# Kernel optimization log

Measured on AMD Instinct MI355X. Metric: run time of the kernel, lower is better.

## Reference

```python
import jax, jax.numpy as jnp
import numpy as np

# Dimensions
MAXN, MAXE = 4096, 8192
B, S, N, E = 8, 512, 1024, 2048
TYPE_DIM, MEM, TENC, EEMB, OUT = 16, 64, 32, 128, 64
MSG = TYPE_DIM + 2 * MEM + TENC + EEMB          # 304: GRU input dim
IN_GNN = EEMB + MEM                              # 192: TransformerConv in_channels
EDGE_DIM = TENC + EEMB                           # 160: TransformerConv edge_dim
# EVENT_TYPE_ID_MAP: pad=0, start=1, end=2, node-add=3, node-delete=4, edge-add=5, edge-delete=6


def setup_inputs() -> dict:
    key = jax.random.key(0)
    ks = jax.random.split(key, 32)
    ri = lambda i, shape, hi: jax.random.randint(ks[i], shape, 0, hi)
    rn = lambda i, shape, s=1.0: jax.random.normal(ks[i], shape, jnp.float32) * s
    ru = lambda i, shape: jax.random.uniform(ks[i], shape, dtype=jnp.float32)
    return {
        "event_type_ids": ri(0, (B, S), 7),
        "src_ids": ri(1, (B, S), MAXN),
        "src_mask": ru(2, (B, S)),
        "dst_ids": ri(3, (B, S), MAXN),
        "dst_mask": ru(4, (B, S)),
        "event_edge_ids": ri(5, (B, S), MAXE),
        "event_embeddings": rn(6, (B, S, EEMB)),
        "event_timestamps": ru(7, (B, S)),
        "node_ids": ri(8, (B, N), MAXN),
        "edge_ids": ri(9, (B, E), MAXE),
        "edge_index": ri(10, (B, 2, E), MAXN),
        "edge_timestamps": ru(11, (B, E)),
        "memory": rn(12, (MAXN, MEM), 0.1),
        "last_update": ru(13, (MAXE,)),
        "node_features": rn(14, (MAXN, EEMB), 0.1),
        "edge_features": rn(15, (MAXE, EEMB), 0.1),
        "type_emb": rn(16, (7, TYPE_DIM), 0.1),
        "time_w": rn(17, (TENC,), 0.1),
        "time_b": rn(18, (TENC,), 0.1),
        "gru_w_ih": rn(19, (3 * MEM, MSG), 0.05),
        "gru_w_hh": rn(20, (3 * MEM, MEM), 0.05),
        "gru_b_ih": rn(21, (3 * MEM,), 0.05),
        "gru_b_hh": rn(22, (3 * MEM,), 0.05),
        "Wq": rn(23, (OUT, IN_GNN), 0.05),
        "bq": rn(24, (OUT,), 0.05),
        "Wk": rn(25, (OUT, IN_GNN), 0.05),
        "bk": rn(26, (OUT,), 0.05),
        "Wv": rn(27, (OUT, IN_GNN), 0.05),
        "bv": rn(28, (OUT,), 0.05),
        "We": rn(29, (OUT, EDGE_DIM), 0.05),
        "Wskip": rn(30, (OUT, IN_GNN), 0.05),
        "bskip": rn(31, (OUT,), 0.05),
    }


def reference(event_type_ids, src_ids, src_mask, dst_ids, dst_mask, event_edge_ids,
              event_embeddings, event_timestamps, node_ids, edge_ids, edge_index,
              edge_timestamps, memory, last_update, node_features, edge_features,
              type_emb, time_w, time_b, gru_w_ih, gru_w_hh, gru_b_ih, gru_b_hh,
              Wq, bq, Wk, bk, Wv, bv, We, Wskip, bskip):
    f32 = jnp.float32
    time_enc = lambda t: jnp.cos(t[..., None] * time_w + time_b)  # TGN TimeEncoder: cos(Linear(t))

    # ---- message() ----
    type_embs = type_emb[event_type_ids]                      # (B,S,TYPE_DIM)
    src_embs = memory[src_ids] * src_mask[..., None]          # (B,S,MEM)
    dst_embs = memory[dst_ids] * dst_mask[..., None]
    rel_edge_ts = event_timestamps - last_update[event_edge_ids] * dst_mask
    is_node_ev = ((event_type_ids == 3) | (event_type_ids == 4)).astype(f32)
    not_special = (event_type_ids >= 3).astype(f32)           # not pad/start/end
    ts_emb = time_enc(event_timestamps * is_node_ev + rel_edge_ts * dst_mask) * not_special[..., None]
    src_msgs = jnp.concatenate([type_embs, src_embs, dst_embs, ts_emb, event_embeddings], -1) * not_special[..., None]
    dst_msgs = jnp.concatenate([type_embs, dst_embs, src_embs, ts_emb, event_embeddings], -1) * dst_mask[..., None]

    # ---- agg_message(): per-batch scatter-mean over node ids ----
    def seg_mean(m, ids):
        s = jax.ops.segment_sum(m, ids, num_segments=MAXN)
        c = jax.ops.segment_sum(jnp.ones(ids.shape, f32), ids, num_segments=MAXN)
        return s / jnp.maximum(c, 1.0)[:, None]
    # after flatten(end_dim=1), gathering by node id < MAXN picks from the batch-0 block
    agg_src0 = jax.vmap(seg_mean)(src_msgs, src_ids)[0]       # (MAXN, MSG)
    agg_dst0 = jax.vmap(seg_mean)(dst_msgs, dst_ids)[0]

    def gru(x, h):
        gi = x @ gru_w_ih.T + gru_b_ih
        gh = h @ gru_w_hh.T + gru_b_hh
        ir, iz, ic = jnp.split(gi, 3, -1)
        hr, hz, hc = jnp.split(gh, 3, -1)
        r = jax.nn.sigmoid(ir + hr)
        z = jax.nn.sigmoid(iz + hz)
        n = jnp.tanh(ic + r * hc)
        return (1.0 - z) * n + z * h

    present_src = jnp.zeros((MAXN,), bool).at[src_ids.ravel()].set(True)
    present_dst = jnp.zeros((MAXN,), bool).at[dst_ids.ravel()].set(True)
    mem_src = gru(agg_src0, memory)
    mem_dst = gru(agg_dst0, memory)
    mem = jnp.where(present_src[:, None], mem_src, memory)
    mem = jnp.where(present_dst[:, None], mem_dst, mem)

    # ---- GNN input prep ----
    rel_t_embs = time_enc(edge_timestamps - last_update[edge_ids])       # (B,E,TENC)
    x = jnp.concatenate([node_features[node_ids], mem[node_ids]], -1).reshape(B * N, IN_GNN)
    # localize_edge_index: first matching position of each edge id in flattened node_ids
    matches = node_ids.ravel()[:, None] == edge_index.ravel()[None, :]   # (B*N, B*2*E) bool
    loc = jnp.argmax(matches, axis=0).reshape(B, 2, E)                   # argmax = first True (0 if none)
    ei = loc.transpose(1, 0, 2).reshape(2, B * E)
    eattr = jnp.concatenate([rel_t_embs, edge_features[edge_ids]], -1).reshape(B * E, EDGE_DIM)

    # ---- TransformerConv (heads=1, root_weight=True, edge_dim set) ----
    q = x @ Wq.T + bq
    k = x @ Wk.T + bk
    v = x @ Wv.T + bv
    e = eattr @ We.T                                                     # lin_edge has no bias in PyG
    src, tgt = ei[0], ei[1]                                              # source_to_target flow
    k_e = k[src] + e
    v_e = v[src] + e
    score = jnp.sum(q[tgt] * k_e, -1) / np.float32(np.sqrt(OUT))
    m = jax.lax.stop_gradient(jax.ops.segment_max(score, tgt, num_segments=B * N))
    p = jnp.exp(score - m[tgt])
    den = jax.ops.segment_sum(p, tgt, num_segments=B * N)
    alpha = p / den[tgt]
    out = jax.ops.segment_sum(alpha[:, None] * v_e, tgt, num_segments=B * N)
    out = out + x @ Wskip.T + bskip
    return out.reshape(B, N, OUT)
```

## Files before the change

kernel.cpp:

```cpp
#include <hip/hip_runtime.h>
#include <math.h>

#define BB 8
#define SS 512
#define NNODE 1024
#define NEDGE 2048
#define MAXN 4096
#define MAXE 8192
#define TYPED 16
#define MEMD 64
#define TENC 32
#define EEMB 128
#define OUTD 64
#define MSG 304
#define INGNN 192
#define EDIM 160
#define BN 8192
#define BE 16384

__device__ __forceinline__ float sigmoidf(float x){ return 1.f/(1.f + expf(-x)); }

__global__ void k_init(float* zero_base, int n_zero, int* first_pos,
                       const float* Wq, const float* Wk, const float* Wv,
                       const float* Wskip, const float* We,
                       const float* bq, const float* bk,
                       const float* bv, const float* bskip,
                       float* WcatT, float* WeT, float* bcat){
  int i = blockIdx.x*blockDim.x + threadIdx.x;
  int stride = gridDim.x*blockDim.x;
  float4* z4 = (float4*)zero_base;
  int n4 = n_zero >> 2;
  float4 zero = {0.f,0.f,0.f,0.f};
  for (int t=i; t<n4; t+=stride) z4[t] = zero;
  for (int t=i; t<MAXN; t+=stride) first_pos[t] = 0x7FFFFFFF;
  int j = i;
  if (j < 4*64*192){
    int o = j/(64*192); int rem = j%(64*192); int q=rem/192, k=rem%192;
    const float* W = (o==0)?Wq:(o==1)?Wk:(o==2)?Wv:Wskip;
    WcatT[k*256 + o*64 + q] = W[rem];
  } else {
    j -= 4*64*192;
    if (j < 64*EDIM){ int q=j/EDIM, k=j%EDIM; WeT[k*64+q] = We[j]; }
    else {
      j -= 64*EDIM;
      if (j < 256){
        const float* b = (j<64)?bq:(j<128)?bk:(j<192)?bv:bskip;
        bcat[j] = b[j&63];
      }
    }
  }
}

__global__ void k_msg_first(const int* ev_type, const int* src_ids, const float* src_mask,
                            const int* dst_ids, const float* dst_mask, const int* ev_edge,
                            const float* ev_emb, const float* ev_ts, const float* memory,
                            const float* last_update, const float* type_emb,
                            const float* time_w, const float* time_b,
                            float* agg_src, float* agg_dst, int* cnt_src, int* cnt_dst,
                            const int* node_ids, int* first_pos, int* ps, int* pd){
  int bb = blockIdx.x;
  if (bb < SS){
    int s = bb;
    int et = ev_type[s];
    int sid = src_ids[s], did = dst_ids[s];
    float sm = src_mask[s], dm = dst_mask[s];
    float ts = ev_ts[s];
    float ns = (et >= 3) ? 1.f : 0.f;
    float ine = (et == 3 || et == 4) ? 1.f : 0.f;
    float rel = ts - last_update[ev_edge[s]] * dm;
    float tin = ts*ine + rel*dm;
    int d = threadIdx.x;
    if (d < MSG){
      float vs, vd;
      if (d < TYPED){ float t = type_emb[et*TYPED + d]; vs = t; vd = t; }
      else if (d < 80){ int c=d-16;  vs = memory[sid*MEMD+c]*sm; vd = memory[did*MEMD+c]*dm; }
      else if (d < 144){ int c=d-80; vs = memory[did*MEMD+c]*dm; vd = memory[sid*MEMD+c]*sm; }
      else if (d < 176){ int c=d-144; float ce = cosf(tin*time_w[c]+time_b[c])*ns; vs=ce; vd=ce; }
      else { float e = ev_emb[s*EEMB + (d-176)]; vs=e; vd=e; }
      atomicAdd(&agg_src[sid*MSG+d], vs*ns);
      atomicAdd(&agg_dst[did*MSG+d], vd*dm);
    }
    if (d == MSG){ atomicAdd(&cnt_src[sid], 1); atomicAdd(&cnt_dst[did], 1); }
  } else {
    int i = (bb - SS)*320 + threadIdx.x;
    if (i < BN) atomicMin(&first_pos[node_ids[i]], i);
    if (i < BB*SS){ ps[src_ids[i]] = 1; pd[dst_ids[i]] = 1; }
  }
}

#define GNT 8
#define GPAD 12
__global__ __launch_bounds__(192) void k_gru(
    const float* agg_src, const float* agg_dst, const int* cnt_src, const int* cnt_dst,
    const int* ps, const int* pd, const float* memory,
    const float* w_ih, const float* w_hh, const float* b_ih, const float* b_hh,
    float* mem_new){
  __shared__ float xs_t[MSG][GPAD];
  __shared__ float hs_t[MEMD][GPAD];
  __shared__ float giL[GNT][192];
  __shared__ float ghL[GNT][192];
  __shared__ int   mode[GNT];
  __shared__ float rcnt[GNT];
  int tid = threadIdx.x;
  int base = blockIdx.x * GNT;
  if (tid < GNT){
    int n = base + tid;
    int m = pd[n] ? 2 : (ps[n] ? 1 : 0);
    mode[tid] = m;
    int c = (m==2) ? cnt_dst[n] : ((m==1) ? cnt_src[n] : 0);
    rcnt[tid] = 1.f / (float)max(c, 1);
  }
  __syncthreads();
  for (int idx = tid; idx < GNT*MSG; idx += 192){
    int t = idx / MSG, k = idx - t*MSG;
    const float* agg = (mode[t]==2) ? agg_dst : agg_src;
    xs_t[k][t] = agg[(base+t)*MSG + k] * rcnt[t];
  }
  for (int idx = tid; idx < GNT*MEMD; idx += 192){
    int t = idx / MEMD, k = idx - t*MEMD;
    hs_t[k][t] = memory[(base+t)*MEMD + k];
  }
  __syncthreads();
  {
    float4 a0 = {0.f,0.f,0.f,0.f}, a1 = {0.f,0.f,0.f,0.f};
    const float* wr = &w_ih[tid*MSG];
    #pragma unroll 2
    for (int k4 = 0; k4 < MSG; k4 += 4){
      float4 w4 = *(const float4*)&wr[k4];
      {
        float4 x0 = *(const float4*)&xs_t[k4][0];
        float4 x1 = *(const float4*)&xs_t[k4][4];
        a0.x += w4.x*x0.x; a0.y += w4.x*x0.y; a0.z += w4.x*x0.z; a0.w += w4.x*x0.w;
        a1.x += w4.x*x1.x; a1.y += w4.x*x1.y; a1.z += w4.x*x1.z; a1.w += w4.x*x1.w;
      }
      {
        float4 x0 = *(const float4*)&xs_t[k4+1][0];
        float4 x1 = *(const float4*)&xs_t[k4+1][4];
        a0.x += w4.y*x0.x; a0.y += w4.y*x0.y; a0.z += w4.y*x0.z; a0.w += w4.y*x0.w;
        a1.x += w4.y*x1.x; a1.y += w4.y*x1.y; a1.z += w4.y*x1.z; a1.w += w4.y*x1.w;
      }
      {
        float4 x0 = *(const float4*)&xs_t[k4+2][0];
        float4 x1 = *(const float4*)&xs_t[k4+2][4];
        a0.x += w4.z*x0.x; a0.y += w4.z*x0.y; a0.z += w4.z*x0.z; a0.w += w4.z*x0.w;
        a1.x += w4.z*x1.x; a1.y += w4.z*x1.y; a1.z += w4.z*x1.z; a1.w += w4.z*x1.w;
      }
      {
        float4 x0 = *(const float4*)&xs_t[k4+3][0];
        float4 x1 = *(const float4*)&xs_t[k4+3][4];
        a0.x += w4.w*x0.x; a0.y += w4.w*x0.y; a0.z += w4.w*x0.z; a0.w += w4.w*x0.w;
        a1.x += w4.w*x1.x; a1.y += w4.w*x1.y; a1.z += w4.w*x1.z; a1.w += w4.w*x1.w;
      }
    }
    float bi = b_ih[tid];
    giL[0][tid]=a0.x+bi; giL[1][tid]=a0.y+bi; giL[2][tid]=a0.z+bi; giL[3][tid]=a0.w+bi;
    giL[4][tid]=a1.x+bi; giL[5][tid]=a1.y+bi; giL[6][tid]=a1.z+bi; giL[7][tid]=a1.w+bi;
  }
  {
    float4 a0 = {0.f,0.f,0.f,0.f}, a1 = {0.f,0.f,0.f,0.f};
    const float* wr = &w_hh[tid*MEMD];
    #pragma unroll 2
    for (int k4 = 0; k4 < MEMD; k4 += 4){
      float4 w4 = *(const float4*)&wr[k4];
      {
        float4 x0 = *(const float4*)&hs_t[k4][0];
        float4 x1 = *(const float4*)&hs_t[k4][4];
        a0.x += w4.x*x0.x; a0.y += w4.x*x0.y; a0.z += w4.x*x0.z; a0.w += w4.x*x0.w;
        a1.x += w4.x*x1.x; a1.y += w4.x*x1.y; a1.z += w4.x*x1.z; a1.w += w4.x*x1.w;
      }
      {
        float4 x0 = *(const float4*)&hs_t[k4+1][0];
        float4 x1 = *(const float4*)&hs_t[k4+1][4];
        a0.x += w4.y*x0.x; a0.y += w4.y*x0.y; a0.z += w4.y*x0.z; a0.w += w4.y*x0.w;
        a1.x += w4.y*x1.x; a1.y += w4.y*x1.y; a1.z += w4.y*x1.z; a1.w += w4.y*x1.w;
      }
      {
        float4 x0 = *(const float4*)&hs_t[k4+2][0];
        float4 x1 = *(const float4*)&hs_t[k4+2][4];
        a0.x += w4.z*x0.x; a0.y += w4.z*x0.y; a0.z += w4.z*x0.z; a0.w += w4.z*x0.w;
        a1.x += w4.z*x1.x; a1.y += w4.z*x1.y; a1.z += w4.z*x1.z; a1.w += w4.z*x1.w;
      }
      {
        float4 x0 = *(const float4*)&hs_t[k4+3][0];
        float4 x1 = *(const float4*)&hs_t[k4+3][4];
        a0.x += w4.w*x0.x; a0.y += w4.w*x0.y; a0.z += w4.w*x0.z; a0.w += w4.w*x0.w;
        a1.x += w4.w*x1.x; a1.y += w4.w*x1.y; a1.z += w4.w*x1.z; a1.w += w4.w*x1.w;
      }
    }
    float bh = b_hh[tid];
    ghL[0][tid]=a0.x+bh; ghL[1][tid]=a0.y+bh; ghL[2][tid]=a0.z+bh; ghL[3][tid]=a0.w+bh;
    ghL[4][tid]=a1.x+bh; ghL[5][tid]=a1.y+bh; ghL[6][tid]=a1.z+bh; ghL[7][tid]=a1.w+bh;
  }
  __syncthreads();
  int cw = tid >> 6, col = tid & 63;
  for (int t = cw; t < GNT; t += 3){
    float h = hs_t[col][t];
    float outv;
    if (mode[t] == 0) outv = h;
    else {
      float r  = sigmoidf(giL[t][col]     + ghL[t][col]);
      float z  = sigmoidf(giL[t][64+col]  + ghL[t][64+col]);
      float ng = tanhf  (giL[t][128+col] + r*ghL[t][128+col]);
      outv = (1.f - z)*ng + z*h;
    }
    mem_new[(base+t)*MEMD + col] = outv;
  }
}

#define QK_CH 96
#define EE_CH 80
__global__ __launch_bounds__(256) void k_mm(
    const int* node_ids, const float* node_feat, const float* mem_new,
    const float* WcatT, const float* bcat,
    float* qbuf, float* kbuf, float* vbuf, float* outbuf,
    const int* edge_ids, const float* edge_ts, const float* last_update,
    const float* edge_features, const float* time_w, const float* time_b,
    const float* WeT, float* ebuf){
  __shared__ float smem[QK_CH*68 + QK_CH*64];
  int tid = threadIdx.x;
  if (blockIdx.x < 512){
    float* xs_t = smem;
    float* wls  = smem + QK_CH*68;
    int rg = blockIdx.x >> 2, cg = blockIdx.x & 3;
    int rbase = rg * 64;
    int rr = tid & 63, qq = tid >> 6;
    int nid = node_ids[rbase + rr];
    int tr = tid >> 4, tc = tid & 15;
    float4 acc[4];
    #pragma unroll
    for (int i=0;i<4;i++) acc[i] = (float4){0.f,0.f,0.f,0.f};
    for (int kc = 0; kc < 2; kc++){
      #pragma unroll 6
      for (int m = 0; m < 24; m++){
        int kk = qq*24 + m;
        int k  = kc*QK_CH + kk;
        float v = (k < EEMB) ? node_feat[nid*EEMB + k] : mem_new[nid*MEMD + (k-EEMB)];
        xs_t[kk*68 + rr] = v;
      }
      #pragma unroll
      for (int it = 0; it < 6; it++){
        int idx = tid + it*256;
        int kk = idx >> 4, c4 = (idx & 15) * 4;
        *(float4*)&wls[kk*64 + c4] = *(const float4*)&WcatT[(kc*QK_CH + kk)*256 + cg*64 + c4];
      }
      __syncthreads();
      #pragma unroll 4
      for (int kk = 0; kk < QK_CH; kk++){
        float4 xv = *(const float4*)&xs_t[kk*68 + tr*4];
        float4 wv = *(const float4*)&wls[kk*64 + tc*4];
        acc[0].x += xv.x*wv.x; acc[0].y += xv.x*wv.y; acc[0].z += xv.x*wv.z; acc[0].w += xv.x*wv.w;
        acc[1].x += xv.y*wv.x; acc[1].y += xv.y*wv.y; acc[1].z += xv.y*wv.z; acc[1].w += xv.y*wv.w;
        acc[2].x += xv.z*wv.x; acc[2].y += xv.z*wv.y; acc[2].z += xv.z*wv.z; acc[2].w += xv.z*wv.w;
        acc[3].x += xv.w*wv.x; acc[3].y += xv.w*wv.y; acc[3].z += xv.w*wv.z; acc[3].w += xv.w*wv.w;
      }
      __syncthreads();
    }
    float4 b4 = *(const float4*)&bcat[cg*64 + tc*4];
    float* dst = (cg==0)? qbuf : (cg==1)? kbuf : (cg==2)? vbuf : outbuf;
    #pragma unroll
    for (int i=0;i<4;i++){
      float4 o = {acc[i].x+b4.x, acc[i].y+b4.y, acc[i].z+b4.z, acc[i].w+b4.w};
      *(float4*)&dst[(rbase + tr*4 + i)*OUTD + tc*4] = o;
    }
  } else {
    float* ea_t = smem;
    float* wls  = smem + EE_CH*68;
    int ebase = (blockIdx.x - 512) * 64;
    int ee = tid & 63, qq = tid >> 6;
    int j = ebase + ee;
    int eid = edge_ids[j];
    float rel = edge_ts[j] - last_update[eid];
    int tr = tid >> 4, tc = tid & 15;
    float4 acc[4];
    #pragma unroll
    for (int i=0;i<4;i++) acc[i] = (float4){0.f,0.f,0.f,0.f};
    for (int kc = 0; kc < 2; kc++){
      #pragma unroll 5
      for (int m = 0; m < 20; m++){
        int kk = qq*20 + m;
        int k  = kc*EE_CH + kk;
        float v = (k < TENC) ? cosf(rel*time_w[k] + time_b[k])
                             : edge_features[eid*EEMB + (k - TENC)];
        ea_t[kk*68 + ee] = v;
      }
      #pragma unroll
      for (int it = 0; it < 5; it++){
        int idx = tid + it*256;
        int kk = idx >> 4, c4 = (idx & 15) * 4;
        *(float4*)&wls[kk*64 + c4] = *(const float4*)&WeT[(kc*EE_CH + kk)*64 + c4];
      }
      __syncthreads();
      #pragma unroll 4
      for (int kk = 0; kk < EE_CH; kk++){
        float4 ev = *(const float4*)&ea_t[kk*68 + tr*4];
        float4 wv = *(const float4*)&wls[kk*64 + tc*4];
        acc[0].x += ev.x*wv.x; acc[0].y += ev.x*wv.y; acc[0].z += ev.x*wv.z; acc[0].w += ev.x*wv.w;
        acc[1].x += ev.y*wv.x; acc[1].y += ev.y*wv.y; acc[1].z += ev.y*wv.z; acc[1].w += ev.y*wv.w;
        acc[2].x += ev.z*wv.x; acc[2].y += ev.z*wv.y; acc[2].z += ev.z*wv.z; acc[2].w += ev.z*wv.w;
        acc[3].x += ev.w*wv.x; acc[3].y += ev.w*wv.y; acc[3].z += ev.w*wv.z; acc[3].w += ev.w*wv.w;
      }
      __syncthreads();
    }
    #pragma unroll
    for (int i=0;i<4;i++)
      *(float4*)&ebuf[(ebase + tr*4 + i)*OUTD + tc*4] = acc[i];
  }
}

__global__ void k_score(const int* edge_index, const int* first_pos,
                        const float* qbuf, const float* kbuf, const float* ebuf,
                        float* pbuf, int* srcpos, int* tgtpos,
                        float* den, float* den0part){
  __shared__ float sden[4];
  int w = threadIdx.x >> 6;
  int j = blockIdx.x*4 + w;
  int c = threadIdx.x & 63;
  int b = j / NEDGE, e = j % NEDGE;
  int vsrc = edge_index[b*2*NEDGE + e];
  int vtgt = edge_index[b*2*NEDGE + NEDGE + e];
  int fs = first_pos[vsrc]; if (fs == 0x7FFFFFFF) fs = 0;
  int ft = first_pos[vtgt]; if (ft == 0x7FFFFFFF) ft = 0;
  float partial = qbuf[ft*OUTD + c] * (kbuf[fs*OUTD + c] + ebuf[j*OUTD + c]);
  #pragma unroll
  for (int off=32; off>0; off>>=1) partial += __shfl_down(partial, off, 64);
  if (c == 0){
    float score = partial * 0.125f;
    float p = expf(score);
    pbuf[j] = p;
    srcpos[j] = fs; tgtpos[j] = ft;
    sden[w] = (ft == 0) ? p : 0.f;
    if (ft != 0) atomicAdd(&den[ft], p);
  }
  __syncthreads();
  if (threadIdx.x == 0) den0part[blockIdx.x] = sden[0]+sden[1]+sden[2]+sden[3];
}

__global__ __launch_bounds__(1024) void k_out(const int* srcpos, const int* tgtpos,
                                              const float* pbuf, const float* den,
                                              const float* vbuf, const float* ebuf,
                                              float* out, float* out0part){
  __shared__ float acc0[16][64];
  int tid = threadIdx.x;
  int w = tid >> 6, c = tid & 63;
  int jbase = blockIdx.x*64 + w*4;
  float a0 = 0.f;
  #pragma unroll
  for (int i=0;i<4;i++){
    int j = jbase + i;
    int ft = tgtpos[j], fs = srcpos[j];
    float p = pbuf[j];
    float ve = vbuf[fs*OUTD + c] + ebuf[j*OUTD + c];
    if (ft == 0) a0 += p * ve;
    else atomicAdd(&out[ft*OUTD + c], (p/den[ft]) * ve);
  }
  acc0[w][c] = a0;
  __syncthreads();
  if (w == 0){
    float t = 0.f;
    #pragma unroll
    for (int i=0;i<16;i++) t += acc0[i][c];
    out0part[blockIdx.x*64 + c] = t;
  }
}

__global__ __launch_bounds__(1024) void k_fin_out(const float* den0part,
                                                  const float* out0part, float* out){
  __shared__ float part[16][64];
  __shared__ float dpart[16];
  __shared__ float s_inv;
  int tid = threadIdx.x;
  int w = tid >> 6, c = tid & 63;
  float d = den0part[tid] + den0part[tid+1024] + den0part[tid+2048] + den0part[tid+3072];
  #pragma unroll
  for (int off=32; off>0; off>>=1) d += __shfl_down(d, off, 64);
  if (c == 0) dpart[w] = d;
  float s = 0.f;
  #pragma unroll
  for (int i=0;i<16;i++) s += out0part[(w + i*16)*64 + c];
  part[w][c] = s;
  __syncthreads();
  if (tid == 0){
    float dt = 0.f;
    #pragma unroll
    for (int i=0;i<16;i++) dt += dpart[i];
    s_inv = (dt > 0.f) ? 1.f/dt : 0.f;
  }
  __syncthreads();
  if (w == 0){
    float t = 0.f;
    #pragma unroll
    for (int i=0;i<16;i++) t += part[i][c];
    out[c] += t * s_inv;
  }
}

extern "C" void kernel_launch(void* const* d_in, const int* in_sizes, int n_in,
                              void* d_out, int out_size, void* d_ws, size_t ws_size,
                              hipStream_t stream){
  const int*   ev_type      = (const int*)  d_in[0];
  const int*   src_ids      = (const int*)  d_in[1];
  const float* src_mask     = (const float*)d_in[2];
  const int*   dst_ids      = (const int*)  d_in[3];
  const float* dst_mask     = (const float*)d_in[4];
  const int*   ev_edge      = (const int*)  d_in[5];
  const float* ev_emb       = (const float*)d_in[6];
  const float* ev_ts        = (const float*)d_in[7];
  const int*   node_ids     = (const int*)  d_in[8];
  const int*   edge_ids     = (const int*)  d_in[9];
  const int*   edge_index   = (const int*)  d_in[10];
  const float* edge_ts      = (const float*)d_in[11];
  const float* memory       = (const float*)d_in[12];
  const float* last_update  = (const float*)d_in[13];
  const float* node_feat    = (const float*)d_in[14];
  const float* edge_feat    = (const float*)d_in[15];
  const float* type_emb     = (const float*)d_in[16];
  const float* time_w       = (const float*)d_in[17];
  const float* time_b       = (const float*)d_in[18];
  const float* gru_w_ih     = (const float*)d_in[19];
  const float* gru_w_hh     = (const float*)d_in[20];
  const float* gru_b_ih     = (const float*)d_in[21];
  const float* gru_b_hh     = (const float*)d_in[22];
  const float* Wq  = (const float*)d_in[23]; const float* bq    = (const float*)d_in[24];
  const float* Wk  = (const float*)d_in[25]; const float* bk    = (const float*)d_in[26];
  const float* Wv  = (const float*)d_in[27]; const float* bv    = (const float*)d_in[28];
  const float* We  = (const float*)d_in[29];
  const float* Wsk = (const float*)d_in[30]; const float* bskip = (const float*)d_in[31];
  float* out = (float*)d_out;

  float* ws = (float*)d_ws;
  size_t off = 0;
  float* agg_src = ws + off; off += (size_t)MAXN*MSG;
  float* agg_dst = ws + off; off += (size_t)MAXN*MSG;
  int* cnt_src   = (int*)(ws + off); off += MAXN;
  int* cnt_dst   = (int*)(ws + off); off += MAXN;
  int* present_s = (int*)(ws + off); off += MAXN;
  int* present_d = (int*)(ws + off); off += MAXN;
  float* den     = ws + off; off += BN;
  int n_zero = (int)off;
  int* first_pos = (int*)(ws + off); off += MAXN;
  float* mem_new = ws + off; off += (size_t)MAXN*MEMD;
  float* qbuf    = ws + off; off += (size_t)BN*OUTD;
  float* kbuf    = ws + off; off += (size_t)BN*OUTD;
  float* vbuf    = ws + off; off += (size_t)BN*OUTD;
  float* ebuf    = ws + off; off += (size_t)BE*OUTD;
  float* pbuf    = ws + off; off += BE;
  int* srcpos    = (int*)(ws + off); off += BE;
  int* tgtpos    = (int*)(ws + off); off += BE;
  float* den0part= ws + off; off += 4096;
  float* out0part= ws + off; off += 256*64;
  float* WcatT   = ws + off; off += (size_t)INGNN*256;
  float* WeT     = ws + off; off += (size_t)EDIM*64;
  float* bcat    = ws + off; off += 256;

  k_init<<<2048, 256, 0, stream>>>(ws, n_zero, first_pos,
                                   Wq, Wk, Wv, Wsk, We, bq, bk, bv, bskip,
                                   WcatT, WeT, bcat);
  k_msg_first<<<SS + (BN + 319)/320, 320, 0, stream>>>(
      ev_type, src_ids, src_mask, dst_ids, dst_mask, ev_edge,
      ev_emb, ev_ts, memory, last_update, type_emb, time_w, time_b,
      agg_src, agg_dst, cnt_src, cnt_dst,
      node_ids, first_pos, present_s, present_d);
  k_gru<<<MAXN/GNT, 192, 0, stream>>>(agg_src, agg_dst, cnt_src, cnt_dst,
                                      present_s, present_d, memory,
                                      gru_w_ih, gru_w_hh, gru_b_ih, gru_b_hh, mem_new);
  k_mm<<<512 + BE/64, 256, 0, stream>>>(node_ids, node_feat, mem_new, WcatT, bcat,
                                        qbuf, kbuf, vbuf, out,
                                        edge_ids, edge_ts, last_update, edge_feat,
                                        time_w, time_b, WeT, ebuf);
  k_score<<<BE/4, 256, 0, stream>>>(edge_index, first_pos, qbuf, kbuf, ebuf,
                                    pbuf, srcpos, tgtpos, den, den0part);
  k_out<<<256, 1024, 0, stream>>>(srcpos, tgtpos, pbuf, den, vbuf, ebuf, out, out0part);
  k_fin_out<<<1, 1024, 0, stream>>>(den0part, out0part, out);
}
```

Measured before the change: 83.97 us.

## Fuse all stages into one cooperative persistent kernel with grid syncs

Replaces the seven-kernel launch chain with a single cooperative kernel of 256 blocks that runs init, message aggregation, GRU, projections, scoring and output phases separated by grid-wide syncs. The score stage now accumulates softmax numerators and denominators directly with atomics into a zeroed num buffer, so the separate output-gather kernel is no longer needed. The aim is to remove kernel launch gaps and one full pass over edges, at the cost of lower parallelism per phase, a larger zeroing region, and grid-sync overhead. The old kernels remain as a fallback if cooperative launch fails.

```diff
diff --git a/kernel.cpp b/kernel.cpp
--- a/kernel.cpp
+++ b/kernel.cpp
@@ -1,5 +1,8 @@
 #include <hip/hip_runtime.h>
+#include <hip/hip_cooperative_groups.h>
 #include <math.h>
+
+namespace cg = cooperative_groups;
 
 #define BB 8
 #define SS 512
@@ -18,9 +21,351 @@
 #define BN 8192
 #define BE 16384
 
+#define GRID 256
+#define TPB 256
+#define QK_CH 96
+#define EE_CH 80
+
 __device__ __forceinline__ float sigmoidf(float x){ return 1.f/(1.f + expf(-x)); }
 
-__global__ void k_init(float* zero_base, int n_zero, int* first_pos,
+struct TgnArgs {
+  const int *ev_type, *src_ids, *dst_ids, *ev_edge, *node_ids, *edge_ids, *edge_index;
+  const float *src_mask, *dst_mask, *ev_emb, *ev_ts, *edge_ts, *memory, *last_update,
+              *node_feat, *edge_feat, *type_emb, *time_w, *time_b,
+              *w_ih, *w_hh, *b_ih, *b_hh,
+              *Wq, *bq, *Wk, *bk, *Wv, *bv, *We, *Wskip, *bskip;
+  float *out;
+  float *agg_src, *agg_dst;
+  int *cnt_src, *cnt_dst, *ps, *pd, *first_pos;
+  float *den, *num, *mem_new, *qbuf, *kbuf, *vbuf, *ebuf,
+        *den0part, *out0part, *WcatT, *WeT, *bcat, *zero_base;
+  int n_zero4;
+};
+
+__global__ __launch_bounds__(TPB) void k_all(TgnArgs A){
+  cg::grid_group grid = cg::this_grid();
+  __shared__ float smem[QK_CH*68 + QK_CH*64];
+  int blk = blockIdx.x, tid = threadIdx.x;
+  int gid = blk*TPB + tid;
+
+  {
+    float4* z4 = (float4*)A.zero_base;
+    float4 zz = {0.f,0.f,0.f,0.f};
+    for (int t = gid; t < A.n_zero4; t += GRID*TPB) z4[t] = zz;
+    for (int t = gid; t < MAXN; t += GRID*TPB) A.first_pos[t] = 0x7FFFFFFF;
+    const int NT1 = 4*64*192, NT2 = 64*EDIM;
+    for (int j = gid; j < NT1 + NT2 + 256; j += GRID*TPB){
+      int jj = j;
+      if (jj < NT1){
+        int o = jj/(64*192); int rem = jj%(64*192); int q = rem/192, k = rem%192;
+        const float* W = (o==0)?A.Wq:(o==1)?A.Wk:(o==2)?A.Wv:A.Wskip;
+        A.WcatT[k*256 + o*64 + q] = W[rem];
+      } else {
+        jj -= NT1;
+        if (jj < NT2){ int q = jj/EDIM, k = jj%EDIM; A.WeT[k*64+q] = A.We[jj]; }
+        else {
+          jj -= NT2;
+          const float* b = (jj<64)?A.bq:(jj<128)?A.bk:(jj<192)?A.bv:A.bskip;
+          A.bcat[jj] = b[jj&63];
+        }
+      }
+    }
+  }
+  grid.sync();
+
+  {
+    for (int s = blk; s < SS; s += GRID){
+      int et = A.ev_type[s];
+      int sid = A.src_ids[s], did = A.dst_ids[s];
+      float sm = A.src_mask[s], dm = A.dst_mask[s];
+      float ts = A.ev_ts[s];
+      float ns = (et >= 3) ? 1.f : 0.f;
+      float ine = (et == 3 || et == 4) ? 1.f : 0.f;
+      float rel = ts - A.last_update[A.ev_edge[s]] * dm;
+      float tin = ts*ine + rel*dm;
+      for (int d = tid; d < MSG; d += TPB){
+        float vs, vd;
+        if (d < TYPED){ float t = A.type_emb[et*TYPED + d]; vs = t; vd = t; }
+        else if (d < 80){ int c=d-16;  vs = A.memory[sid*MEMD+c]*sm; vd = A.memory[did*MEMD+c]*dm; }
+        else if (d < 144){ int c=d-80; vs = A.memory[did*MEMD+c]*dm; vd = A.memory[sid*MEMD+c]*sm; }
+        else if (d < 176){ int c=d-144; float ce = cosf(tin*A.time_w[c]+A.time_b[c])*ns; vs=ce; vd=ce; }
+        else { float e = A.ev_emb[s*EEMB + (d-176)]; vs=e; vd=e; }
+        atomicAdd(&A.agg_src[sid*MSG+d], vs*ns);
+        atomicAdd(&A.agg_dst[did*MSG+d], vd*dm);
+      }
+      if (tid == 0){ atomicAdd(&A.cnt_src[sid], 1); atomicAdd(&A.cnt_dst[did], 1); }
+    }
+    for (int i = gid; i < BN; i += GRID*TPB){
+      atomicMin(&A.first_pos[A.node_ids[i]], i);
+      if (i < BB*SS){ A.ps[A.src_ids[i]] = 1; A.pd[A.dst_ids[i]] = 1; }
+    }
+  }
+  grid.sync();
+
+  for (int base = blk*8; base < MAXN; base += GRID*8){
+    float* xs_t = smem;
+    float* hs_t = smem + 3648;
+    float* giL  = smem + 4416;
+    float* ghL  = smem + 5952;
+    int*   mode = (int*)(smem + 7488);
+    float* rcnt = smem + 7496;
+    if (tid < 8){
+      int n = base + tid;
+      int m = A.pd[n] ? 2 : (A.ps[n] ? 1 : 0);
+      mode[tid] = m;
+      int c = (m==2) ? A.cnt_dst[n] : ((m==1) ? A.cnt_src[n] : 0);
+      rcnt[tid] = 1.f / (float)max(c, 1);
+    }
+    __syncthreads();
+    for (int idx = tid; idx < 8*MSG; idx += TPB){
+      int t = idx / MSG, k = idx - t*MSG;
+      const float* agg = (mode[t]==2) ? A.agg_dst : A.agg_src;
+      xs_t[k*12 + t] = agg[(base+t)*MSG + k] * rcnt[t];
+    }
+    for (int idx = tid; idx < 8*MEMD; idx += TPB){
+      int t = idx / MEMD, k = idx - t*MEMD;
+      hs_t[k*12 + t] = A.memory[(base+t)*MEMD + k];
+    }
+    __syncthreads();
+    if (tid < 192){
+      float4 a0={0,0,0,0}, a1={0,0,0,0};
+      const float* wr = &A.w_ih[tid*MSG];
+      #pragma unroll 2
+      for (int k4 = 0; k4 < MSG; k4 += 4){
+        float4 w4 = *(const float4*)&wr[k4];
+        float4 x0, x1;
+        x0 = *(const float4*)&xs_t[(k4+0)*12]; x1 = *(const float4*)&xs_t[(k4+0)*12+4];
+        a0.x += w4.x*x0.x; a0.y += w4.x*x0.y; a0.z += w4.x*x0.z; a0.w += w4.x*x0.w;
+        a1.x += w4.x*x1.x; a1.y += w4.x*x1.y; a1.z += w4.x*x1.z; a1.w += w4.x*x1.w;
+        x0 = *(const float4*)&xs_t[(k4+1)*12]; x1 = *(const float4*)&xs_t[(k4+1)*12+4];
+        a0.x += w4.y*x0.x; a0.y += w4.y*x0.y; a0.z += w4.y*x0.z; a0.w += w4.y*x0.w;
+        a1.x += w4.y*x1.x; a1.y += w4.y*x1.y; a1.z += w4.y*x1.z; a1.w += w4.y*x1.w;
+        x0 = *(const float4*)&xs_t[(k4+2)*12]; x1 = *(const float4*)&xs_t[(k4+2)*12+4];
+        a0.x += w4.z*x0.x; a0.y += w4.z*x0.y; a0.z += w4.z*x0.z; a0.w += w4.z*x0.w;
+        a1.x += w4.z*x1.x; a1.y += w4.z*x1.y; a1.z += w4.z*x1.z; a1.w += w4.z*x1.w;
+        x0 = *(const float4*)&xs_t[(k4+3)*12]; x1 = *(const float4*)&xs_t[(k4+3)*12+4];
+        a0.x += w4.w*x0.x; a0.y += w4.w*x0.y; a0.z += w4.w*x0.z; a0.w += w4.w*x0.w;
+        a1.x += w4.w*x1.x; a1.y += w4.w*x1.y; a1.z += w4.w*x1.z; a1.w += w4.w*x1.w;
+      }
+      float bi = A.b_ih[tid];
+      giL[0*192+tid]=a0.x+bi; giL[1*192+tid]=a0.y+bi; giL[2*192+tid]=a0.z+bi; giL[3*192+tid]=a0.w+bi;
+      giL[4*192+tid]=a1.x+bi; giL[5*192+tid]=a1.y+bi; giL[6*192+tid]=a1.z+bi; giL[7*192+tid]=a1.w+bi;
+      float4 b0={0,0,0,0}, b1={0,0,0,0};
+      const float* wh = &A.w_hh[tid*MEMD];
+      #pragma unroll 2
+      for (int k4 = 0; k4 < MEMD; k4 += 4){
+        float4 w4 = *(const float4*)&wh[k4];
+        float4 x0, x1;
+        x0 = *(const float4*)&hs_t[(k4+0)*12]; x1 = *(const float4*)&hs_t[(k4+0)*12+4];
+        b0.x += w4.x*x0.x; b0.y += w4.x*x0.y; b0.z += w4.x*x0.z; b0.w += w4.x*x0.w;
+        b1.x += w4.x*x1.x; b1.y += w4.x*x1.y; b1.z += w4.x*x1.z; b1.w += w4.x*x1.w;
+        x0 = *(const float4*)&hs_t[(k4+1)*12]; x1 = *(const float4*)&hs_t[(k4+1)*12+4];
+        b0.x += w4.y*x0.x; b0.y += w4.y*x0.y; b0.z += w4.y*x0.z; b0.w += w4.y*x0.w;
+        b1.x += w4.y*x1.x; b1.y += w4.y*x1.y; b1.z += w4.y*x1.z; b1.w += w4.y*x1.w;
+        x0 = *(const float4*)&hs_t[(k4+2)*12]; x1 = *(const float4*)&hs_t[(k4+2)*12+4];
+        b0.x += w4.z*x0.x; b0.y += w4.z*x0.y; b0.z += w4.z*x0.z; b0.w += w4.z*x0.w;
+        b1.x += w4.z*x1.x; b1.y += w4.z*x1.y; b1.z += w4.z*x1.z; b1.w += w4.z*x1.w;
+        x0 = *(const float4*)&hs_t[(k4+3)*12]; x1 = *(const float4*)&hs_t[(k4+3)*12+4];
+        b0.x += w4.w*x0.x; b0.y += w4.w*x0.y; b0.z += w4.w*x0.z; b0.w += w4.w*x0.w;
+        b1.x += w4.w*x1.x; b1.y += w4.w*x1.y; b1.z += w4.w*x1.z; b1.w += w4.w*x1.w;
+      }
+      float bh = A.b_hh[tid];
+      ghL[0*192+tid]=b0.x+bh; ghL[1*192+tid]=b0.y+bh; ghL[2*192+tid]=b0.z+bh; ghL[3*192+tid]=b0.w+bh;
+      ghL[4*192+tid]=b1.x+bh; ghL[5*192+tid]=b1.y+bh; ghL[6*192+tid]=b1.z+bh; ghL[7*192+tid]=b1.w+bh;
+    }
+    __syncthreads();
+    int cw = tid >> 6, col = tid & 63;
+    for (int t = cw; t < 8; t += 4){
+      float h = hs_t[col*12 + t];
+      float outv;
+      int m = mode[t];
+      if (m == 0) outv = h;
+      else {
+        float r  = sigmoidf(giL[t*192+col]      + ghL[t*192+col]);
+        float z  = sigmoidf(giL[t*192+64+col]   + ghL[t*192+64+col]);
+        float ng = tanhf  (giL[t*192+128+col] + r*ghL[t*192+128+col]);
+        outv = (1.f - z)*ng + z*h;
+      }
+      A.mem_new[(base+t)*MEMD + col] = outv;
+    }
+    __syncthreads();
+  }
+  grid.sync();
+
+  for (int unit = blk; unit < 768; unit += GRID){
+    if (unit < 512){
+      float* xs_t = smem;
+      float* wls  = smem + QK_CH*68;
+      int rg = unit >> 2, cgx = unit & 3;
+      int rbase = rg * 64;
+      int rr = tid & 63, qq = tid >> 6;
+      int nid = A.node_ids[rbase + rr];
+      int tr = tid >> 4, tc = tid & 15;
+      float4 acc[4];
+      #pragma unroll
+      for (int i=0;i<4;i++) acc[i] = (float4){0.f,0.f,0.f,0.f};
+      for (int kc = 0; kc < 2; kc++){
+        #pragma unroll 6
+        for (int m = 0; m < 24; m++){
+          int kk = qq*24 + m;
+          int k  = kc*QK_CH + kk;
+          float v = (k < EEMB) ? A.node_feat[nid*EEMB + k] : A.mem_new[nid*MEMD + (k-EEMB)];
+          xs_t[kk*68 + rr] = v;
+        }
+        #pragma unroll
+        for (int it = 0; it < 6; it++){
+          int idx = tid + it*256;
+          int kk = idx >> 4, c4 = (idx & 15) * 4;
+          *(float4*)&wls[kk*64 + c4] = *(const float4*)&A.WcatT[(kc*QK_CH + kk)*256 + cgx*64 + c4];
+        }
+        __syncthreads();
+        #pragma unroll 4
+        for (int kk = 0; kk < QK_CH; kk++){
+          float4 xv = *(const float4*)&xs_t[kk*68 + tr*4];
+          float4 wv = *(const float4*)&wls[kk*64 + tc*4];
+          acc[0].x += xv.x*wv.x; acc[0].y += xv.x*wv.y; acc[0].z += xv.x*wv.z; acc[0].w += xv.x*wv.w;
+          acc[1].x += xv.y*wv.x; acc[1].y += xv.y*wv.y; acc[1].z += xv.y*wv.z; acc[1].w += xv.y*wv.w;
+          acc[2].x += xv.z*wv.x; acc[2].y += xv.z*wv.y; acc[2].z += xv.z*wv.z; acc[2].w += xv.z*wv.w;
+          acc[3].x += xv.w*wv.x; acc[3].y += xv.w*wv.y; acc[3].z += xv.w*wv.z; acc[3].w += xv.w*wv.w;
+        }
+        __syncthreads();
+      }
+      float4 b4 = *(const float4*)&A.bcat[cgx*64 + tc*4];
+      float* dst = (cgx==0)? A.qbuf : (cgx==1)? A.kbuf : (cgx==2)? A.vbuf : A.out;
+      #pragma unroll
+      for (int i=0;i<4;i++){
+        float4 o = {acc[i].x+b4.x, acc[i].y+b4.y, acc[i].z+b4.z, acc[i].w+b4.w};
+        *(float4*)&dst[(rbase + tr*4 + i)*OUTD + tc*4] = o;
+      }
+    } else {
+      float* ea_t = smem;
+      float* wls  = smem + EE_CH*68;
+      int ebase = (unit - 512) * 64;
+      int ee = tid & 63, qq = tid >> 6;
+      int j = ebase + ee;
+      int eid = A.edge_ids[j];
+      float rel = A.edge_ts[j] - A.last_update[eid];
+      int tr = tid >> 4, tc = tid & 15;
+      float4 acc[4];
+      #pragma unroll
+      for (int i=0;i<4;i++) acc[i] = (float4){0.f,0.f,0.f,0.f};
+      for (int kc = 0; kc < 2; kc++){
+        #pragma unroll 5
+        for (int m = 0; m < 20; m++){
+          int kk = qq*20 + m;
+          int k  = kc*EE_CH + kk;
+          float v = (k < TENC) ? cosf(rel*A.time_w[k] + A.time_b[k])
+                               : A.edge_feat[eid*EEMB + (k - TENC)];
+          ea_t[kk*68 + ee] = v;
+        }
+        #pragma unroll
+        for (int it = 0; it < 5; it++){
+          int idx = tid + it*256;
+          int kk = idx >> 4, c4 = (idx & 15) * 4;
+          *(float4*)&wls[kk*64 + c4] = *(const float4*)&A.WeT[(kc*EE_CH + kk)*64 + c4];
+        }
+        __syncthreads();
+        #pragma unroll 4
+        for (int kk = 0; kk < EE_CH; kk++){
+          float4 ev = *(const float4*)&ea_t[kk*68 + tr*4];
+          float4 wv = *(const float4*)&wls[kk*64 + tc*4];
+          acc[0].x += ev.x*wv.x; acc[0].y += ev.x*wv.y; acc[0].z += ev.x*wv.z; acc[0].w += ev.x*wv.w;
+          acc[1].x += ev.y*wv.x; acc[1].y += ev.y*wv.y; acc[1].z += ev.y*wv.z; acc[1].w += ev.y*wv.w;
+          acc[2].x += ev.z*wv.x; acc[2].y += ev.z*wv.y; acc[2].z += ev.z*wv.z; acc[2].w += ev.z*wv.w;
+          acc[3].x += ev.w*wv.x; acc[3].y += ev.w*wv.y; acc[3].z += ev.w*wv.z; acc[3].w += ev.w*wv.w;
+        }
+        __syncthreads();
+      }
+      #pragma unroll
+      for (int i=0;i<4;i++)
+        *(float4*)&A.ebuf[(ebase + tr*4 + i)*OUTD + tc*4] = acc[i];
+    }
+  }
+  grid.sync();
+
+  {
+    float* acc0 = smem;
+    float* sdw  = smem + 256;
+    int w = tid >> 6, c = tid & 63;
+    for (int chunk = blk; chunk < 1024; chunk += GRID){
+      float a0 = 0.f, pden = 0.f;
+      #pragma unroll
+      for (int u = 0; u < 4; u++){
+        int j = chunk*16 + w*4 + u;
+        int b = j >> 11, e = j & 2047;
+        int vsrc = A.edge_index[b*2*NEDGE + e];
+        int vtgt = A.edge_index[b*2*NEDGE + NEDGE + e];
+        int fs = A.first_pos[vsrc]; if (fs == 0x7FFFFFFF) fs = 0;
+        int ft = A.first_pos[vtgt]; if (ft == 0x7FFFFFFF) ft = 0;
+        float ej = A.ebuf[j*OUTD + c];
+        float partial = A.qbuf[ft*OUTD + c] * (A.kbuf[fs*OUTD + c] + ej);
+        #pragma unroll
+        for (int off = 32; off > 0; off >>= 1) partial += __shfl_down(partial, off, 64);
+        float sc = __shfl(partial, 0, 64);
+        float pe = expf(sc * 0.125f);
+        float ve = A.vbuf[fs*OUTD + c] + ej;
+        if (ft == 0){ a0 += pe*ve; pden += pe; }
+        else {
+          atomicAdd(&A.num[ft*OUTD + c], pe*ve);
+          if (c == 0) atomicAdd(&A.den[ft], pe);
+        }
+      }
+      acc0[w*64 + c] = a0;
+      if (c == 0) sdw[w] = pden;
+      __syncthreads();
+      if (w == 0){
+        float t4 = acc0[c] + acc0[64+c] + acc0[128+c] + acc0[192+c];
+        A.out0part[chunk*64 + c] = t4;
+        if (c == 0) A.den0part[chunk] = sdw[0]+sdw[1]+sdw[2]+sdw[3];
+      }
+      __syncthreads();
+    }
+  }
+  grid.sync();
+
+  for (int unit = blk; unit < 516; unit += GRID){
+    if (unit < 512){
+      int r = unit*16 + (tid >> 4);
+      int c4 = (tid & 15) * 4;
+      if (r > 0){
+        float d = A.den[r];
+        if (d > 0.f){
+          float rinv = 1.f / d;
+          float4 n4 = *(const float4*)&A.num[r*64 + c4];
+          float4 o4 = *(const float4*)&A.out[r*64 + c4];
+          o4.x += n4.x*rinv; o4.y += n4.y*rinv; o4.z += n4.z*rinv; o4.w += n4.w*rinv;
+          *(float4*)&A.out[r*64 + c4] = o4;
+        }
+      }
+    } else {
+      float* sdata = smem;
+      float* dred  = smem + 256;
+      int cbase = (unit - 512) * 16;
+      int ci = tid >> 4, ch = tid & 15;
+      int c = cbase + ci;
+      float s = 0.f;
+      for (int j = ch*64; j < ch*64 + 64; j++) s += A.out0part[j*64 + c];
+      sdata[ci*16 + ch] = s;
+      float dd = A.den0part[tid] + A.den0part[tid+256] + A.den0part[tid+512] + A.den0part[tid+768];
+      #pragma unroll
+      for (int off = 32; off > 0; off >>= 1) dd += __shfl_down(dd, off, 64);
+      if ((tid & 63) == 0) dred[tid >> 6] = dd;
+      __syncthreads();
+      if (tid == 0) smem[260] = dred[0]+dred[1]+dred[2]+dred[3];
+      __syncthreads();
+      if (ch == 0){
+        float den0 = smem[260];
+        float tot = 0.f;
+        #pragma unroll
+        for (int q = 0; q < 16; q++) tot += sdata[ci*16 + q];
+        if (den0 > 0.f) A.out[c] += tot / den0;
+      }
+      __syncthreads();
+    }
+  }
+}
+
+__global__ void f_init(float* zero_base, int n_zero, int* first_pos,
                        const float* Wq, const float* Wk, const float* Wv,
                        const float* Wskip, const float* We,
                        const float* bq, const float* bk,
@@ -51,7 +396,7 @@
   }
 }
 
-__global__ void k_msg_first(const int* ev_type, const int* src_ids, const float* src_mask,
+__global__ void f_msg_first(const int* ev_type, const int* src_ids, const float* src_mask,
                             const int* dst_ids, const float* dst_mask, const int* ev_edge,
                             const float* ev_emb, const float* ev_ts, const float* memory,
                             const float* last_update, const float* type_emb,
@@ -89,14 +434,13 @@
 }
 
 #define GNT 8
-#define GPAD 12
-__global__ __launch_bounds__(192) void k_gru(
+__global__ __launch_bounds__(192) void f_gru(
     const float* agg_src, const float* agg_dst, const int* cnt_src, const int* cnt_dst,
     const int* ps, const int* pd, const float* memory,
     const float* w_ih, const float* w_hh, const float* b_ih, const float* b_hh,
     float* mem_new){
-  __shared__ float xs_t[MSG][GPAD];
-  __shared__ float hs_t[MEMD][GPAD];
+  __shared__ float xs_t[MSG][12];
+  __shared__ float hs_t[MEMD][12];
   __shared__ float giL[GNT][192];
   __shared__ float ghL[GNT][192];
   __shared__ int   mode[GNT];
@@ -122,70 +466,48 @@
   }
   __syncthreads();
   {
-    float4 a0 = {0.f,0.f,0.f,0.f}, a1 = {0.f,0.f,0.f,0.f};
+    float4 a0 = {0,0,0,0}, a1 = {0,0,0,0};
     const float* wr = &w_ih[tid*MSG];
     #pragma unroll 2
     for (int k4 = 0; k4 < MSG; k4 += 4){
       float4 w4 = *(const float4*)&wr[k4];
-      {
-        float4 x0 = *(const float4*)&xs_t[k4][0];
-        float4 x1 = *(const float4*)&xs_t[k4][4];
-        a0.x += w4.x*x0.x; a0.y += w4.x*x0.y; a0.z += w4.x*x0.z; a0.w += w4.x*x0.w;
-        a1.x += w4.x*x1.x; a1.y += w4.x*x1.y; a1.z += w4.x*x1.z; a1.w += w4.x*x1.w;
-      }
-      {
-        float4 x0 = *(const float4*)&xs_t[k4+1][0];
-        float4 x1 = *(const float4*)&xs_t[k4+1][4];
-        a0.x += w4.y*x0.x; a0.y += w4.y*x0.y; a0.z += w4.y*x0.z; a0.w += w4.y*x0.w;
-        a1.x += w4.y*x1.x; a1.y += w4.y*x1.y; a1.z += w4.y*x1.z; a1.w += w4.y*x1.w;
-      }
-      {
-        float4 x0 = *(const float4*)&xs_t[k4+2][0];
-        float4 x1 = *(const float4*)&xs_t[k4+2][4];
-        a0.x += w4.z*x0.x; a0.y += w4.z*x0.y; a0.z += w4.z*x0.z; a0.w += w4.z*x0.w;
-        a1.x += w4.z*x1.x; a1.y += w4.z*x1.y; a1.z += w4.z*x1.z; a1.w += w4.z*x1.w;
-      }
-      {
-        float4 x0 = *(const float4*)&xs_t[k4+3][0];
-        float4 x1 = *(const float4*)&xs_t[k4+3][4];
-        a0.x += w4.w*x0.x; a0.y += w4.w*x0.y; a0.z += w4.w*x0.z; a0.w += w4.w*x0.w;
-        a1.x += w4.w*x1.x; a1.y += w4.w*x1.y; a1.z += w4.w*x1.z; a1.w += w4.w*x1.w;
-      }
+      float4 x0, x1;
+      x0 = *(const float4*)&xs_t[k4+0][0]; x1 = *(const float4*)&xs_t[k4+0][4];
+      a0.x += w4.x*x0.x; a0.y += w4.x*x0.y; a0.z += w4.x*x0.z; a0.w += w4.x*x0.w;
+      a1.x += w4.x*x1.x; a1.y += w4.x*x1.y; a1.z += w4.x*x1.z; a1.w += w4.x*x1.w;
+      x0 = *(const float4*)&xs_t[k4+1][0]; x1 = *(const float4*)&xs_t[k4+1][4];
+      a0.x += w4.y*x0.x; a0.y += w4.y*x0.y; a0.z += w4.y*x0.z; a0.w += w4.y*x0.w;
+      a1.x += w4.y*x1.x; a1.y += w4.y*x1.y; a1.z += w4.y*x1.z; a1.w += w4.y*x1.w;
+      x0 = *(const float4*)&xs_t[k4+2][0]; x1 = *(const float4*)&xs_t[k4+2][4];
+      a0.x += w4.z*x0.x; a0.y += w4.z*x0.y; a0.z += w4.z*x0.z; a0.w += w4.z*x0.w;
+      a1.x += w4.z*x1.x; a1.y += w4.z*x1.y; a1.z += w4.z*x1.z; a1.w += w4.z*x1.w;
+      x0 = *(const float4*)&xs_t[k4+3][0]; x1 = *(const float4*)&xs_t[k4+3][4];
+      a0.x += w4.w*x0.x; a0.y += w4.w*x0.y; a0.z += w4.w*x0.z; a0.w += w4.w*x0.w;
+      a1.x += w4.w*x1.x; a1.y += w4.w*x1.y; a1.z += w4.w*x1.z; a1.w += w4.w*x1.w;
     }
     float bi = b_ih[tid];
     giL[0][tid]=a0.x+bi; giL[1][tid]=a0.y+bi; giL[2][tid]=a0.z+bi; giL[3][tid]=a0.w+bi;
     giL[4][tid]=a1.x+bi; giL[5][tid]=a1.y+bi; giL[6][tid]=a1.z+bi; giL[7][tid]=a1.w+bi;
   }
   {
-    float4 a0 = {0.f,0.f,0.f,0.f}, a1 = {0.f,0.f,0.f,0.f};
+    float4 a0 = {0,0,0,0}, a1 = {0,0,0,0};
     const float* wr = &w_hh[tid*MEMD];
     #pragma unroll 2
     for (int k4 = 0; k4 < MEMD; k4 += 4){
       float4 w4 = *(const float4*)&wr[k4];
-      {
-        float4 x0 = *(const float4*)&hs_t[k4][0];
-        float4 x1 = *(const float4*)&hs_t[k4][4];
-        a0.x += w4.x*x0.x; a0.y += w4.x*x0.y; a0.z += w4.x*x0.z; a0.w += w4.x*x0.w;
-        a1.x += w4.x*x1.x; a1.y += w4.x*x1.y; a1.z += w4.x*x1.z; a1.w += w4.x*x1.w;
-      }
-      {
-        float4 x0 = *(const float4*)&hs_t[k4+1][0];
-        float4 x1 = *(const float4*)&hs_t[k4+1][4];
-        a0.x += w4.y*x0.x; a0.y += w4.y*x0.y; a0.z += w4.y*x0.z; a0.w += w4.y*x0.w;
-        a1.x += w4.y*x1.x; a1.y += w4.y*x1.y; a1.z += w4.y*x1.z; a1.w += w4.y*x1.w;
-      }
-      {
-        float4 x0 = *(const float4*)&hs_t[k4+2][0];
-        float4 x1 = *(const float4*)&hs_t[k4+2][4];
-        a0.x += w4.z*x0.x; a0.y += w4.z*x0.y; a0.z += w4.z*x0.z; a0.w += w4.z*x0.w;
-        a1.x += w4.z*x1.x; a1.y += w4.z*x1.y; a1.z += w4.z*x1.z; a1.w += w4.z*x1.w;
-      }
-      {
-        float4 x0 = *(const float4*)&hs_t[k4+3][0];
-        float4 x1 = *(const float4*)&hs_t[k4+3][4];
-        a0.x += w4.w*x0.x; a0.y += w4.w*x0.y; a0.z += w4.w*x0.z; a0.w += w4.w*x0.w;
-        a1.x += w4.w*x1.x; a1.y += w4.w*x1.y; a1.z += w4.w*x1.z; a1.w += w4.w*x1.w;
-      }
+      float4 x0, x1;
+      x0 = *(const float4*)&hs_t[k4+0][0]; x1 = *(const float4*)&hs_t[k4+0][4];
+      a0.x += w4.x*x0.x; a0.y += w4.x*x0.y; a0.z += w4.x*x0.z; a0.w += w4.x*x0.w;
+      a1.x += w4.x*x1.x; a1.y += w4.x*x1.y; a1.z += w4.x*x1.z; a1.w += w4.x*x1.w;
+      x0 = *(const float4*)&hs_t[k4+1][0]; x1 = *(const float4*)&hs_t[k4+1][4];
+      a0.x += w4.y*x0.x; a0.y += w4.y*x0.y; a0.z += w4.y*x0.z; a0.w += w4.y*x0.w;
+      a1.x += w4.y*x1.x; a1.y += w4.y*x1.y; a1.z += w4.y*x1.z; a1.w += w4.y*x1.w;
+      x0 = *(const float4*)&hs_t[k4+2][0]; x1 = *(const float4*)&hs_t[k4+2][4];
+      a0.x += w4.z*x0.x; a0.y += w4.z*x0.y; a0.z += w4.z*x0.z; a0.w += w4.z*x0.w;
+      a1.x += w4.z*x1.x; a1.y += w4.z*x1.y; a1.z += w4.z*x1.z; a1.w += w4.z*x1.w;
+      x0 = *(const float4*)&hs_t[k4+3][0]; x1 = *(const float4*)&hs_t[k4+3][4];
+      a0.x += w4.w*x0.x; a0.y += w4.w*x0.y; a0.z += w4.w*x0.z; a0.w += w4.w*x0.w;
+      a1.x += w4.w*x1.x; a1.y += w4.w*x1.y; a1.z += w4.w*x1.z; a1.w += w4.w*x1.w;
     }
     float bh = b_hh[tid];
     ghL[0][tid]=a0.x+bh; ghL[1][tid]=a0.y+bh; ghL[2][tid]=a0.z+bh; ghL[3][tid]=a0.w+bh;
@@ -207,9 +529,7 @@
   }
 }
 
-#define QK_CH 96
-#define EE_CH 80
-__global__ __launch_bounds__(256) void k_mm(
+__global__ __launch_bounds__(256) void f_mm(
     const int* node_ids, const float* node_feat, const float* mem_new,
     const float* WcatT, const float* bcat,
     float* qbuf, float* kbuf, float* vbuf, float* outbuf,
@@ -221,7 +541,7 @@
   if (blockIdx.x < 512){
     float* xs_t = smem;
     float* wls  = smem + QK_CH*68;
-    int rg = blockIdx.x >> 2, cg = blockIdx.x & 3;
+    int rg = blockIdx.x >> 2, cgx = blockIdx.x & 3;
     int rbase = rg * 64;
     int rr = tid & 63, qq = tid >> 6;
     int nid = node_ids[rbase + rr];
@@ -241,7 +561,7 @@
       for (int it = 0; it < 6; it++){
         int idx = tid + it*256;
         int kk = idx >> 4, c4 = (idx & 15) * 4;
-        *(float4*)&wls[kk*64 + c4] = *(const float4*)&WcatT[(kc*QK_CH + kk)*256 + cg*64 + c4];
+        *(float4*)&wls[kk*64 + c4] = *(const float4*)&WcatT[(kc*QK_CH + kk)*256 + cgx*64 + c4];
       }
       __syncthreads();
       #pragma unroll 4
@@ -255,8 +575,8 @@
       }
       __syncthreads();
     }
-    float4 b4 = *(const float4*)&bcat[cg*64 + tc*4];
-    float* dst = (cg==0)? qbuf : (cg==1)? kbuf : (cg==2)? vbuf : outbuf;
+    float4 b4 = *(const float4*)&bcat[cgx*64 + tc*4];
+    float* dst = (cgx==0)? qbuf : (cgx==1)? kbuf : (cgx==2)? vbuf : outbuf;
     #pragma unroll
     for (int i=0;i<4;i++){
       float4 o = {acc[i].x+b4.x, acc[i].y+b4.y, acc[i].z+b4.z, acc[i].w+b4.w};
@@ -307,7 +627,7 @@
   }
 }
 
-__global__ void k_score(const int* edge_index, const int* first_pos,
+__global__ void f_score(const int* edge_index, const int* first_pos,
                         const float* qbuf, const float* kbuf, const float* ebuf,
                         float* pbuf, int* srcpos, int* tgtpos,
                         float* den, float* den0part){
@@ -335,7 +655,7 @@
   if (threadIdx.x == 0) den0part[blockIdx.x] = sden[0]+sden[1]+sden[2]+sden[3];
 }
 
-__global__ __launch_bounds__(1024) void k_out(const int* srcpos, const int* tgtpos,
+__global__ __launch_bounds__(1024) void f_out(const int* srcpos, const int* tgtpos,
                                               const float* pbuf, const float* den,
                                               const float* vbuf, const float* ebuf,
                                               float* out, float* out0part){
@@ -363,7 +683,7 @@
   }
 }
 
-__global__ __launch_bounds__(1024) void k_fin_out(const float* den0part,
+__global__ __launch_bounds__(1024) void f_fin_out(const float* den0part,
                                                   const float* out0part, float* out){
   __shared__ float part[16][64];
   __shared__ float dpart[16];
@@ -397,78 +717,91 @@
 extern "C" void kernel_launch(void* const* d_in, const int* in_sizes, int n_in,
                               void* d_out, int out_size, void* d_ws, size_t ws_size,
                               hipStream_t stream){
-  const int*   ev_type      = (const int*)  d_in[0];
-  const int*   src_ids      = (const int*)  d_in[1];
-  const float* src_mask     = (const float*)d_in[2];
-  const int*   dst_ids      = (const int*)  d_in[3];
-  const float* dst_mask     = (const float*)d_in[4];
-  const int*   ev_edge      = (const int*)  d_in[5];
-  const float* ev_emb       = (const float*)d_in[6];
-  const float* ev_ts        = (const float*)d_in[7];
-  const int*   node_ids     = (const int*)  d_in[8];
-  const int*   edge_ids     = (const int*)  d_in[9];
-  const int*   edge_index   = (const int*)  d_in[10];
-  const float* edge_ts      = (const float*)d_in[11];
-  const float* memory       = (const float*)d_in[12];
-  const float* last_update  = (const float*)d_in[13];
-  const float* node_feat    = (const float*)d_in[14];
-  const float* edge_feat    = (const float*)d_in[15];
-  const float* type_emb     = (const float*)d_in[16];
-  const float* time_w       = (const float*)d_in[17];
-  const float* time_b       = (const float*)d_in[18];
-  const float* gru_w_ih     = (const float*)d_in[19];
-  const float* gru_w_hh     = (const float*)d_in[20];
-  const float* gru_b_ih     = (const float*)d_in[21];
-  const float* gru_b_hh     = (const float*)d_in[22];
-  const float* Wq  = (const float*)d_in[23]; const float* bq    = (const float*)d_in[24];
-  const float* Wk  = (const float*)d_in[25]; const float* bk    = (const float*)d_in[26];
-  const float* Wv  = (const float*)d_in[27]; const float* bv    = (const float*)d_in[28];
-  const float* We  = (const float*)d_in[29];
-  const float* Wsk = (const float*)d_in[30]; const float* bskip = (const float*)d_in[31];
-  float* out = (float*)d_out;
+  TgnArgs A;
+  A.ev_type     = (const int*)  d_in[0];
+  A.src_ids     = (const int*)  d_in[1];
+  A.src_mask    = (const float*)d_in[2];
+  A.dst_ids     = (const int*)  d_in[3];
+  A.dst_mask    = (const float*)d_in[4];
+  A.ev_edge     = (const int*)  d_in[5];
+  A.ev_emb      = (const float*)d_in[6];
+  A.ev_ts       = (const float*)d_in[7];
+  A.node_ids    = (const int*)  d_in[8];
+  A.edge_ids    = (const int*)  d_in[9];
+  A.edge_index  = (const int*)  d_in[10];
+  A.edge_ts     = (const float*)d_in[11];
+  A.memory      = (const float*)d_in[12];
+  A.last_update = (const float*)d_in[13];
+  A.node_feat   = (const float*)d_in[14];
+  A.edge_feat   = (const float*)d_in[15];
+  A.type_emb    = (const float*)d_in[16];
+  A.time_w      = (const float*)d_in[17];
+  A.time_b      = (const float*)d_in[18];
+  A.w_ih        = (const float*)d_in[19];
+  A.w_hh        = (const float*)d_in[20];
+  A.b_ih        = (const float*)d_in[21];
+  A.b_hh        = (const float*)d_in[22];
+  A.Wq = (const float*)d_in[23]; A.bq = (const float*)d_in[24];
+  A.Wk = (const float*)d_in[25]; A.bk = (const float*)d_in[26];
+  A.Wv = (const float*)d_in[27]; A.bv = (const float*)d_in[28];
+  A.We = (const float*)d_in[29];
+  A.Wskip = (const float*)d_in[30]; A.bskip = (const float*)d_in[31];
+  A.out = (float*)d_out;
 
   float* ws = (float*)d_ws;
   size_t off = 0;
-  float* agg_src = ws + off; off += (size_t)MAXN*MSG;
-  float* agg_dst = ws + off; off += (size_t)MAXN*MSG;
-  int* cnt_src   = (int*)(ws + off); off += MAXN;
-  int* cnt_dst   = (int*)(ws + off); off += MAXN;
-  int* present_s = (int*)(ws + off); off += MAXN;
-  int* present_d = (int*)(ws + off); off += MAXN;
-  float* den     = ws + off; off += BN;
+  A.zero_base = ws;
+  A.agg_src = ws + off; off += (size_t)MAXN*MSG;
+  A.agg_dst = ws + off; off += (size_t)MAXN*MSG;
+  A.cnt_src = (int*)(ws + off); off += MAXN;
+  A.cnt_dst = (int*)(ws + off); off += MAXN;
+  A.ps      = (int*)(ws + off); off += MAXN;
+  A.pd      = (int*)(ws + off); off += MAXN;
+  A.den     = ws + off; off += BN;
+  A.num     = ws + off; off += (size_t)BN*OUTD;
   int n_zero = (int)off;
-  int* first_pos = (int*)(ws + off); off += MAXN;
-  float* mem_new = ws + off; off += (size_t)MAXN*MEMD;
-  float* qbuf    = ws + off; off += (size_t)BN*OUTD;
-  float* kbuf    = ws + off; off += (size_t)BN*OUTD;
-  float* vbuf    = ws + off; off += (size_t)BN*OUTD;
-  float* ebuf    = ws + off; off += (size_t)BE*OUTD;
-  float* pbuf    = ws + off; off += BE;
-  int* srcpos    = (int*)(ws + off); off += BE;
-  int* tgtpos    = (int*)(ws + off); off += BE;
-  float* den0part= ws + off; off += 4096;
-  float* out0part= ws + off; off += 256*64;
-  float* WcatT   = ws + off; off += (size_t)INGNN*256;
-  float* WeT     = ws + off; off += (size_t)EDIM*64;
-  float* bcat    = ws + off; off += 256;
-
-  k_init<<<2048, 256, 0, stream>>>(ws, n_zero, first_pos,
-                                   Wq, Wk, Wv, Wsk, We, bq, bk, bv, bskip,
-                                   WcatT, WeT, bcat);
-  k_msg_first<<<SS + (BN + 319)/320, 320, 0, stream>>>(
-      ev_type, src_ids, src_mask, dst_ids, dst_mask, ev_edge,
-      ev_emb, ev_ts, memory, last_update, type_emb, time_w, time_b,
-      agg_src, agg_dst, cnt_src, cnt_dst,
-      node_ids, first_pos, present_s, present_d);
-  k_gru<<<MAXN/GNT, 192, 0, stream>>>(agg_src, agg_dst, cnt_src, cnt_dst,
-                                      present_s, present_d, memory,
-                                      gru_w_ih, gru_w_hh, gru_b_ih, gru_b_hh, mem_new);
-  k_mm<<<512 + BE/64, 256, 0, stream>>>(node_ids, node_feat, mem_new, WcatT, bcat,
-                                        qbuf, kbuf, vbuf, out,
-                                        edge_ids, edge_ts, last_update, edge_feat,
-                                        time_w, time_b, WeT, ebuf);
-  k_score<<<BE/4, 256, 0, stream>>>(edge_index, first_pos, qbuf, kbuf, ebuf,
-                                    pbuf, srcpos, tgtpos, den, den0part);
-  k_out<<<256, 1024, 0, stream>>>(srcpos, tgtpos, pbuf, den, vbuf, ebuf, out, out0part);
-  k_fin_out<<<1, 1024, 0, stream>>>(den0part, out0part, out);
+  A.n_zero4 = n_zero >> 2;
+  A.first_pos = (int*)(ws + off); off += MAXN;
+  A.mem_new   = ws + off; off += (size_t)MAXN*MEMD;
+  A.qbuf      = ws + off; off += (size_t)BN*OUTD;
+  A.kbuf      = ws + off; off += (size_t)BN*OUTD;
+  A.vbuf      = ws + off; off += (size_t)BN*OUTD;
+  A.ebuf      = ws + off; off += (size_t)BE*OUTD;
+  A.den0part  = ws + off; off += 1024;
+  A.out0part  = ws + off; off += 1024*64;
+  float* pbuf      = ws + off; off += BE;
+  int*   srcpos    = (int*)(ws + off); off += BE;
+  int*   tgtpos    = (int*)(ws + off); off += BE;
+  float* den0part7 = ws + off; off += 4096;
+  float* out0part7 = ws + off; off += 256*64;
+  A.WcatT     = ws + off; off += (size_t)INGNN*256;
+  A.WeT       = ws + off; off += (size_t)EDIM*64;
+  A.bcat      = ws + off; off += 256;
+
+  void* args[] = { (void*)&A };
+  hipError_t err = hipLaunchCooperativeKernel((const void*)k_all, dim3(GRID), dim3(TPB),
+                                              args, 0, stream);
+  if (err != hipSuccess){
+    f_init<<<2048, 256, 0, stream>>>(ws, n_zero, A.first_pos,
+                                     A.Wq, A.Wk, A.Wv, A.Wskip, A.We,
+                                     A.bq, A.bk, A.bv, A.bskip,
+                                     A.WcatT, A.WeT, A.bcat);
+    f_msg_first<<<SS + (BN + 319)/320, 320, 0, stream>>>(
+        A.ev_type, A.src_ids, A.src_mask, A.dst_ids, A.dst_mask, A.ev_edge,
+        A.ev_emb, A.ev_ts, A.memory, A.last_update, A.type_emb, A.time_w, A.time_b,
+        A.agg_src, A.agg_dst, A.cnt_src, A.cnt_dst,
+        A.node_ids, A.first_pos, A.ps, A.pd);
+    f_gru<<<MAXN/GNT, 192, 0, stream>>>(A.agg_src, A.agg_dst, A.cnt_src, A.cnt_dst,
+                                        A.ps, A.pd, A.memory,
+                                        A.w_ih, A.w_hh, A.b_ih, A.b_hh, A.mem_new);
+    f_mm<<<512 + BE/64, 256, 0, stream>>>(A.node_ids, A.node_feat, A.mem_new, A.WcatT, A.bcat,
+                                          A.qbuf, A.kbuf, A.vbuf, A.out,
+                                          A.edge_ids, A.edge_ts, A.last_update, A.edge_feat,
+                                          A.time_w, A.time_b, A.WeT, A.ebuf);
+    f_score<<<BE/4, 256, 0, stream>>>(A.edge_index, A.first_pos, A.qbuf, A.kbuf, A.ebuf,
+                                      pbuf, srcpos, tgtpos, A.den, den0part7);
+    f_out<<<256, 1024, 0, stream>>>(srcpos, tgtpos, pbuf, A.den, A.vbuf, A.ebuf,
+                                    A.out, out0part7);
+    f_fin_out<<<1, 1024, 0, stream>>>(den0part7, out0part7, A.out);
+  }
 }
```

Result: slower. 279.3 us (+232.6%).
